# Kernel optimization log

Hardware: AMD Instinct MI355X
Metric: run time of the kernel (lower is better)

## Reference

```python
import jax, jax.numpy as jnp
import numpy as np

# ---- module hyperparameters (from init_kwargs) ----
FREQ_RANGE = (100.0, 8000.0)
CHANNELS = 128
BW_FACTOR = 1.0
SAMPLE_RATE = 16000
ORDER = 4                    # gammatone order (4 cascaded one-pole sections)
ATT_HALF_BW_DB = -3.0        # pyfilterbank default attenuation at half bandwidth


def _hertz_to_erbscale(f):
    return 21.4 * np.log10(4.37e-3 * f + 1.0)


def _erbscale_to_hertz(e):
    return (10.0 ** (e / 21.4) - 1.0) / 4.37e-3


def _design_bank():
    """Replicates pyfilterbank.gammatone: frequencies_gammatone_bank + design_filter.
    normfreq=0 so the ERB offset term is zero."""
    sb = _hertz_to_erbscale(FREQ_RANGE[0])
    eb = _hertz_to_erbscale(FREQ_RANGE[1])
    density = (eb - sb) / (CHANNELS - 0.05)
    cf = _erbscale_to_hertz(np.arange(sb, eb, density))        # [C] center freqs (Hz)
    erb_aud = 24.7 * (4.37e-3 * cf + 1.0)                      # audiological ERB
    phi = np.pi * BW_FACTOR * erb_aud / SAMPLE_RATE
    alpha = 10.0 ** (0.1 * ATT_HALF_BW_DB / ORDER)
    p = (-2.0 + 2.0 * alpha * np.cos(phi)) / (1.0 - alpha)
    lam = -p / 2.0 - np.sqrt(p * p / 4.0 - 1.0)
    beta = 2.0 * np.pi * cf / SAMPLE_RATE
    coef = lam * np.exp(1j * beta)                             # complex pole [C]
    factor = 2.0 * (1.0 - np.abs(coef)) ** ORDER               # stage-1 gain [C]
    return coef, factor


def setup_inputs() -> dict:
    key = jax.random.key(0)
    inp = jax.random.normal(key, (8, 32000), dtype=jnp.float32)  # [B, T] waveforms
    coef, factor = _design_bank()
    return {
        "inp": inp,
        "coef_re": jnp.asarray(np.real(coef), dtype=jnp.float32),  # [C]
        "coef_im": jnp.asarray(np.imag(coef), dtype=jnp.float32),  # [C]
        "factor": jnp.asarray(factor, dtype=jnp.float32),          # [C]
    }


def reference(inp, coef_re, coef_im, factor):
    """Gammatone filterbank analysis: 4 cascaded complex one-pole IIR sections
    per band, applied to every (batch, band) pair in parallel; returns the real
    part, shaped [B, T, C] like the original module's np stacking/transpose."""
    coef = (coef_re + 1j * coef_im).astype(jnp.complex64)          # [C]
    B, T = inp.shape
    C = coef.shape[0]
    # time-major stage input: [T, B, C]; stage 1 applies the gain `factor`
    y = inp.T[:, :, None].astype(jnp.complex64) * factor.astype(jnp.complex64)
    s0 = jnp.zeros((B, C), dtype=jnp.complex64)

    def one_pole(x):
        # s[t] = coef * s[t-1] + x[t], zero initial state (lfilter zi=0)
        def step(s, xt):
            s = coef * s + xt
            return s, s
        _, out = jax.lax.scan(step, s0, x)
        return out

    for _ in range(ORDER):   # fixed small cascade, stages 2..4 have b0 = 1
        y = one_pole(y)
    return jnp.real(y).transpose(1, 0, 2).astype(jnp.float32)      # [B, T, C]
```

## Files before the change

### kernel.cpp

```cpp
#include <hip/hip_runtime.h>


typedef float f32x2 __attribute__((ext_vector_type(2)));

#define B_N    8
#define T_LEN  32000
#define C_CH   128
#define L_CHK  500
#define NB     64
#define W_MAX  1024

#define CSTEP(XR) do {                              \
    const f32x2 xin = {(XR), 0.f};                  \
    f32x2 t;                                        \
    t = crr * s1 + xin;  s1 = cni * s1.yx + t;      \
    t = crr * s2 + s1;   s2 = cni * s2.yx + t;      \
    t = crr * s3 + s2;   s3 = cni * s3.yx + t;      \
    t = crr * s4 + s3;   s4 = cni * s4.yx + t;      \
} while (0)

__global__ __launch_bounds__(64) void gt_trunc(
    const float* __restrict__ x, const float* __restrict__ cre,
    const float* __restrict__ cim, const float* __restrict__ fac,
    float* __restrict__ out)
{
    __shared__ __align__(16) float xs[L_CHK + W_MAX + 4];
    const int g  = blockIdx.x;
    const int k  = blockIdx.y;
    const int b  = blockIdx.z;
    const int c  = g * 64 + threadIdx.x;
    const int t0 = k * L_CHK;

    const float cr0 = cre[g * 64], ci0 = cim[g * 64];
    const float negln = -0.5f * __logf(cr0 * cr0 + ci0 * ci0);
    int W = (int)ceilf(18.0f / negln) + 2;
    W = (W + 3) & ~3;
    if (W > W_MAX) W = W_MAX;
    int start = t0 - W;
    if (start < 0) start = 0;
    const int n  = t0 + L_CHK - start;
    const int nw = t0 - start;

    const float* xb = x + (size_t)b * T_LEN + start;
    for (int i = threadIdx.x; i < n; i += 64) xs[i] = xb[i];

    const float cr = cre[c], ci = cim[c], f = fac[c];
    const f32x2 crr = {cr, cr};
    const f32x2 cni = {-ci, ci};
    __syncthreads();

    f32x2 s1 = {0.f, 0.f}, s2 = {0.f, 0.f}, s3 = {0.f, 0.f}, s4 = {0.f, 0.f};

    float4 cur = *(const float4*)&xs[0];
    for (int i = 0; i < nw; i += 4) {
        const float4 nxt = *(const float4*)&xs[i + 4];
        CSTEP(cur.x); CSTEP(cur.y); CSTEP(cur.z); CSTEP(cur.w);
        cur = nxt;
    }

    float* op = out + ((size_t)b * T_LEN + t0) * C_CH + c;
    for (int j = 0; j < L_CHK; j += 4) {
        const float4 nxt = *(const float4*)&xs[nw + j + 4];
        CSTEP(cur.x); op[(size_t)(j + 0) * C_CH] = s4.x * f;
        CSTEP(cur.y); op[(size_t)(j + 1) * C_CH] = s4.x * f;
        CSTEP(cur.z); op[(size_t)(j + 2) * C_CH] = s4.x * f;
        CSTEP(cur.w); op[(size_t)(j + 3) * C_CH] = s4.x * f;
        cur = nxt;
    }
}

extern "C" void kernel_launch(void* const* d_in, const int* in_sizes, int n_in,
                              void* d_out, int out_size, void* d_ws, size_t ws_size,
                              hipStream_t stream) {
    const float* x   = (const float*)d_in[0];
    const float* cre = (const float*)d_in[1];
    const float* cim = (const float*)d_in[2];
    const float* fac = (const float*)d_in[3];
    float* out = (float*)d_out;

    gt_trunc<<<dim3(2, NB, B_N), 64, 0, stream>>>(x, cre, cim, fac, out);
}
```

Baseline: 159.9 us.

## Skew the four-stage IIR cascade into a software pipeline to break dependency chain

Each time step previously ran the four one-pole sections serially, so every section waited on the one before it. The cascade is now skewed: each section updates from the previous section's state one step earlier, so all four updates in a step are independent and can issue together. A short prologue computes the initial skewed states from the first three inputs, and the shared-memory input is shifted by one slot with zero padding at the end. The output index bookkeeping changes to match, which risks off-by-one errors at chunk edges.

Measured after the change: 152.2 us. -4.8%, faster.

```diff
diff --git a/kernel.cpp b/kernel.cpp
--- a/kernel.cpp
+++ b/kernel.cpp
@@ -10,13 +10,16 @@
 #define NB     64
 #define W_MAX  1024
 
-#define CSTEP(XR) do {                              \
-    const f32x2 xin = {(XR), 0.f};                  \
-    f32x2 t;                                        \
-    t = crr * s1 + xin;  s1 = cni * s1.yx + t;      \
-    t = crr * s2 + s1;   s2 = cni * s2.yx + t;      \
-    t = crr * s3 + s2;   s3 = cni * s3.yx + t;      \
-    t = crr * s4 + s3;   s4 = cni * s4.yx + t;      \
+#define PSTEP(XR) do {                               \
+    const f32x2 xin = {(XR), 0.f};                   \
+    const f32x2 t4 = crr * s4 + s3;                  \
+    const f32x2 t3 = crr * s3 + s2;                  \
+    const f32x2 t2 = crr * s2 + s1;                  \
+    const f32x2 t1 = crr * s1 + xin;                 \
+    s4 = cni * s4.yx + t4;                           \
+    s3 = cni * s3.yx + t3;                           \
+    s2 = cni * s2.yx + t2;                           \
+    s1 = cni * s1.yx + t1;                           \
 } while (0)
 
 __global__ __launch_bounds__(64) void gt_trunc(
@@ -24,7 +27,7 @@
     const float* __restrict__ cim, const float* __restrict__ fac,
     float* __restrict__ out)
 {
-    __shared__ __align__(16) float xs[L_CHK + W_MAX + 4];
+    __shared__ __align__(16) float xs[L_CHK + W_MAX + 8];
     const int g  = blockIdx.x;
     const int k  = blockIdx.y;
     const int b  = blockIdx.z;
@@ -42,29 +45,37 @@
     const int nw = t0 - start;
 
     const float* xb = x + (size_t)b * T_LEN + start;
-    for (int i = threadIdx.x; i < n; i += 64) xs[i] = xb[i];
+    for (int i = threadIdx.x; i < n; i += 64) xs[i + 1] = xb[i];
+    if (threadIdx.x < 7) xs[n + 1 + threadIdx.x] = 0.f;
 
     const float cr = cre[c], ci = cim[c], f = fac[c];
     const f32x2 crr = {cr, cr};
     const f32x2 cni = {-ci, ci};
     __syncthreads();
 
-    f32x2 s1 = {0.f, 0.f}, s2 = {0.f, 0.f}, s3 = {0.f, 0.f}, s4 = {0.f, 0.f};
+    const f32x2 a0 = {xs[1], 0.f}, a1 = {xs[2], 0.f}, a2 = {xs[3], 0.f};
+    f32x2 t, y11, s1, s2, s3, s4;
+    t  = crr * a0  + a1;  y11 = cni * a0.yx  + t;
+    t  = crr * y11 + a2;  s1  = cni * y11.yx + t;
+    t  = crr * a0  + y11; s2  = cni * a0.yx  + t;
+    s3 = a0;
+    s4 = (f32x2){0.f, 0.f};
 
-    float4 cur = *(const float4*)&xs[0];
+    float4 cur = *(const float4*)&xs[4];
     for (int i = 0; i < nw; i += 4) {
-        const float4 nxt = *(const float4*)&xs[i + 4];
-        CSTEP(cur.x); CSTEP(cur.y); CSTEP(cur.z); CSTEP(cur.w);
+        const float4 nxt = *(const float4*)&xs[i + 8];
+        PSTEP(cur.x); PSTEP(cur.y); PSTEP(cur.z); PSTEP(cur.w);
         cur = nxt;
     }
 
     float* op = out + ((size_t)b * T_LEN + t0) * C_CH + c;
-    for (int j = 0; j < L_CHK; j += 4) {
-        const float4 nxt = *(const float4*)&xs[nw + j + 4];
-        CSTEP(cur.x); op[(size_t)(j + 0) * C_CH] = s4.x * f;
-        CSTEP(cur.y); op[(size_t)(j + 1) * C_CH] = s4.x * f;
-        CSTEP(cur.z); op[(size_t)(j + 2) * C_CH] = s4.x * f;
-        CSTEP(cur.w); op[(size_t)(j + 3) * C_CH] = s4.x * f;
+    for (int i = nw; i < nw + L_CHK; i += 4) {
+        const float4 nxt = *(const float4*)&xs[i + 8];
+        PSTEP(cur.x); op[0 * C_CH] = s4.x * f;
+        PSTEP(cur.y); op[1 * C_CH] = s4.x * f;
+        PSTEP(cur.z); op[2 * C_CH] = s4.x * f;
+        PSTEP(cur.w); op[3 * C_CH] = s4.x * f;
+        op += 4 * (size_t)C_CH;
         cur = nxt;
     }
 }
```
